# Performance work log

Measured on AMD Instinct MI355X. Metric: run time of the kernel, lower is better.

The kernel has to match this reference:

```python
import jax, jax.numpy as jnp
import numpy as np

DIM = 1024
HEADS = 16
DIM_HEAD = DIM // HEADS  # 64
MAX_FREQ = 256


def rotate_half(x):
    # interleaved pairs: (..., d) -> rotate each (x1, x2) pair to (-x2, x1)
    x = x.reshape(*x.shape[:-1], -1, 2)
    x1, x2 = x[..., 0], x[..., 1]
    return jnp.stack([-x2, x1], axis=-1).reshape(*x.shape[:-2], -1)


def axial_freqs_2d(H, W, rot_dim, max_freq):
    # 'pixel' freqs: linspace(1, max_freq/2, n) * pi per axis; each axis gets rot_dim/2 rotary dims
    n = rot_dim // 4
    freqs = jnp.linspace(1.0, max_freq / 2.0, n, dtype=jnp.float32) * jnp.pi
    ph = jnp.linspace(-1.0, 1.0, H, dtype=jnp.float32)
    pw = jnp.linspace(-1.0, 1.0, W, dtype=jnp.float32)
    fh = jnp.repeat(ph[:, None] * freqs[None, :], 2, axis=-1)  # (H, rot_dim//2)
    fw = jnp.repeat(pw[:, None] * freqs[None, :], 2, axis=-1)  # (W, rot_dim//2)
    fh = jnp.broadcast_to(fh[:, None, :], (H, W, rot_dim // 2))
    fw = jnp.broadcast_to(fw[None, :, :], (H, W, rot_dim // 2))
    return jnp.concatenate([fh, fw], axis=-1)  # (H, W, rot_dim)


def setup_inputs() -> dict:
    key = jax.random.key(0)
    k1, k2, k3 = jax.random.split(key, 3)
    b, H, W = 8, 32, 32
    L = H * W
    x = jax.random.normal(k1, (b, L, DIM), dtype=jnp.float32)
    # torch Linear weights stored pre-transposed for direct x @ W
    w_qkv = jax.random.normal(k2, (DIM, 3 * DIM), dtype=jnp.float32) * (DIM ** -0.5)
    w_proj = jax.random.normal(k3, (DIM, DIM), dtype=jnp.float32) * (DIM ** -0.5)
    return {"x": x, "w_qkv": w_qkv, "w_proj": w_proj, "H": H, "W": W}


def reference(x, w_qkv, w_proj, H, W):
    b, L, d = x.shape
    qkv = x @ w_qkv  # (b, L, 3d)
    q, k, v = jnp.split(qkv, 3, axis=-1)

    def split_heads(t):
        return t.reshape(b, L, HEADS, DIM_HEAD)  # (b, L, h, dh)

    q, k, v = split_heads(q), split_heads(k), split_heads(v)

    # 2D axial RoPE over the full head dim (rope_use_dim == dim_head)
    freqs = axial_freqs_2d(H, W, DIM_HEAD, MAX_FREQ).reshape(L, DIM_HEAD)
    cos = jnp.cos(freqs)[None, :, None, :]  # (1, L, 1, dh)
    sin = jnp.sin(freqs)[None, :, None, :]
    q = q * cos + rotate_half(q) * sin
    k = k * cos + rotate_half(k) * sin

    # module pre-scales q by dh^-0.5 AND SDPA scales again by dh^-0.5 -> dh^-1 total (faithful)
    scale_total = 1.0 / DIM_HEAD
    scores = jnp.einsum('blhd,bmhd->bhlm', q, k) * scale_total  # (b, h, L, L)
    attn = jax.nn.softmax(scores, axis=-1)
    out = jnp.einsum('bhlm,bmhd->blhd', attn, v).reshape(b, L, d)
    return out @ w_proj
```

## Files before the change

kernel.cpp:

```cpp
#include <hip/hip_runtime.h>
#include <hip/hip_bf16.h>
#include <math.h>

typedef __bf16 bf16_t;
typedef __attribute__((ext_vector_type(8))) __bf16 bf16x8;
typedef __attribute__((ext_vector_type(4))) __bf16 bf16x4;
typedef __attribute__((ext_vector_type(4))) short s16x4;
typedef __attribute__((ext_vector_type(4))) float f32x4;

#define AS1C(p) ((const __attribute__((address_space(1))) void*)(p))
#define AS3(p)  ((__attribute__((address_space(3))) void*)(p))

__device__ __forceinline__ float fast_exp2(float x) { return __builtin_amdgcn_exp2f(x); }

__global__ __launch_bounds__(256) void k_cvt(const float* __restrict__ in,
                                             bf16_t* __restrict__ out, int n4) {
    int i = blockIdx.x * 256 + threadIdx.x;
    if (i < n4) {
        float4 v = reinterpret_cast<const float4*>(in)[i];
        bf16x4 o;
        o[0] = (bf16_t)v.x; o[1] = (bf16_t)v.y; o[2] = (bf16_t)v.z; o[3] = (bf16_t)v.w;
        reinterpret_cast<bf16x4*>(out)[i] = o;
    }
}

__global__ __launch_bounds__(256) void k_tconv(const float* __restrict__ in,
                                               bf16_t* __restrict__ out, int R, int C) {
    __shared__ float tile[64][65];
    int r0 = blockIdx.y * 64, c0 = blockIdx.x * 64;
#pragma unroll
    for (int i = 0; i < 16; ++i) {
        int e = i * 256 + threadIdx.x;
        int r = e >> 6, c = e & 63;
        tile[r][c] = in[(size_t)(r0 + r) * C + c0 + c];
    }
    __syncthreads();
#pragma unroll
    for (int i = 0; i < 16; ++i) {
        int e = i * 256 + threadIdx.x;
        int c = e >> 6, r = e & 63;
        out[(size_t)(c0 + c) * R + r0 + r] = (bf16_t)tile[r][c];
    }
}

__global__ __launch_bounds__(256) void k_tab(float* __restrict__ cosT,
                                             float* __restrict__ sinT) {
    int i = blockIdx.x * 256 + threadIdx.x;
    int l = i >> 6, d = i & 63;
    int hh = l >> 5, ww = l & 31;
    float pos = (d < 32) ? (-1.0f + (2.0f / 31.0f) * (float)hh)
                         : (-1.0f + (2.0f / 31.0f) * (float)ww);
    int fi = (d & 31) >> 1;
    float fb = (1.0f + (127.0f / 15.0f) * (float)fi) * 3.14159265358979323846f;
    float fr = pos * fb;
    cosT[i] = cosf(fr);
    sinT[i] = sinf(fr);
}

__device__ __forceinline__ void gemm128_pipe(const bf16_t* __restrict__ A,
                                             const bf16_t* __restrict__ Bt,
                                             int rowA0, int colB0, int w, int l,
                                             bf16_t* As, bf16_t* Bs,
                                             f32x4 acc[4][4]) {
    const int wr = w >> 1, wc = w & 1;
    const int r8 = l >> 3;
    const int sc = ((l & 7) ^ r8) << 3;

#define STG8(buf, kt)                                                                      \
    {                                                                                      \
        _Pragma("unroll")                                                                  \
        for (int j = 0; j < 4; ++j) {                                                      \
            int rr = j * 32 + w * 8 + r8;                                                  \
            __builtin_amdgcn_global_load_lds(                                              \
                AS1C(A + (size_t)(rowA0 + rr) * 1024 + (kt) * 64 + sc),                    \
                AS3(As + (buf) * 8192 + (j * 32 + w * 8) * 64), 16, 0, 0);                 \
            __builtin_amdgcn_global_load_lds(                                              \
                AS1C(Bt + (size_t)(colB0 + rr) * 1024 + (kt) * 64 + sc),                   \
                AS3(Bs + (buf) * 8192 + (j * 32 + w * 8) * 64), 16, 0, 0);                 \
        }                                                                                  \
    }

    STG8(0, 0);
    for (int T = 0; T < 16; ++T) {
        if (T < 15) {
            STG8((T + 1) & 1, T + 1);
            asm volatile("s_waitcnt vmcnt(8)" ::: "memory");
        } else {
            asm volatile("s_waitcnt vmcnt(0)" ::: "memory");
        }
        __builtin_amdgcn_s_barrier();
        const bf16_t* cA = As + (T & 1) * 8192;
        const bf16_t* cB = Bs + (T & 1) * 8192;
#pragma unroll
        for (int kk = 0; kk < 2; ++kk) {
            const int ec = (kk * 32 + (l >> 4) * 8) ^ ((l & 7) << 3);
            bf16x8 af[4], bfr[4];
#pragma unroll
            for (int mm = 0; mm < 4; ++mm)
                af[mm] = *reinterpret_cast<const bf16x8*>(
                    cA + (wr * 64 + mm * 16 + (l & 15)) * 64 + ec);
#pragma unroll
            for (int n = 0; n < 4; ++n)
                bfr[n] = *reinterpret_cast<const bf16x8*>(
                    cB + (wc * 64 + n * 16 + (l & 15)) * 64 + ec);
            asm volatile("s_waitcnt lgkmcnt(0)" ::: "memory");
            __builtin_amdgcn_sched_barrier(0);
            __builtin_amdgcn_s_setprio(1);
#pragma unroll
            for (int mm = 0; mm < 4; ++mm)
#pragma unroll
                for (int n = 0; n < 4; ++n)
                    acc[mm][n] = __builtin_amdgcn_mfma_f32_16x16x32_bf16(af[mm], bfr[n],
                                                                         acc[mm][n], 0, 0, 0);
            __builtin_amdgcn_s_setprio(0);
        }
        __builtin_amdgcn_s_barrier();
    }
#undef STG8
}

__global__ __launch_bounds__(256, 2) void k_gemm_qkv(const bf16_t* __restrict__ A,
                                                     const bf16_t* __restrict__ Bt,
                                                     const float* __restrict__ cosT,
                                                     const float* __restrict__ sinT,
                                                     bf16_t* __restrict__ qb,
                                                     bf16_t* __restrict__ kb,
                                                     bf16_t* __restrict__ vb) {
    __shared__ alignas(128) char smem[65536];
    bf16_t* As = (bf16_t*)smem;
    bf16_t* Bs = (bf16_t*)(smem + 32768);
    const int tid = threadIdx.x, w = tid >> 6, l = tid & 63;
    const int wr = w >> 1, wc = w & 1;
    const int bid = blockIdx.x;
    const int xcd = bid & 7, idx = bid >> 3;
    const int by = (xcd >> 1) * 16 + (idx & 15);
    const int bx = (xcd & 1) * 12 + (idx >> 4);
    const int rowA0 = by * 128, colB0 = bx * 128;

    f32x4 acc[4][4] = {};
    gemm128_pipe(A, Bt, rowA0, colB0, w, l, As, Bs, acc);

    const int part = colB0 >> 10;
    if (part == 2) {
        __builtin_amdgcn_sched_barrier(0);
        __syncthreads();
        bf16_t* Tb = (bf16_t*)smem;
#pragma unroll
        for (int m = 0; m < 4; ++m)
#pragma unroll
            for (int n = 0; n < 4; ++n) {
                int cc = wc * 64 + n * 16 + (l & 15);
                int rr = wr * 64 + m * 16 + (l >> 4) * 4;
#pragma unroll
                for (int r = 0; r < 4; ++r)
                    Tb[cc * 136 + rr + r] = (bf16_t)acc[m][n][r];
            }
        __syncthreads();
        const int j = tid >> 1, half = tid & 1;
        const int c = colB0 + j;
        const int head = (c & 1023) >> 6, d = c & 63;
        const int bb = rowA0 >> 10, ll0 = rowA0 & 1023;
        bf16_t* dst = vb + (((size_t)bb * 16 + head) * 64 + d) * 1024 + ll0 + half * 64;
        const bf16_t* srcp = Tb + j * 136 + half * 64;
#pragma unroll
        for (int e = 0; e < 8; ++e)
            *reinterpret_cast<bf16x8*>(dst + e * 8) =
                *reinterpret_cast<const bf16x8*>(srcp + e * 8);
    } else {
        bf16_t* dstb = (part == 0) ? qb : kb;
#pragma unroll
        for (int m = 0; m < 4; ++m)
#pragma unroll
            for (int n = 0; n < 4; ++n) {
                const int c = colB0 + wc * 64 + n * 16 + (l & 15);
                const int head = (c & 1023) >> 6;
                const int d = c & 63;
                const int rbase = rowA0 + wr * 64 + m * 16 + (l >> 4) * 4;
#pragma unroll
                for (int r = 0; r < 4; ++r) {
                    int row = rbase + r;
                    int bb = row >> 10, ll = row & 1023;
                    float v0 = acc[m][n][r];
                    float vp = __shfl_xor(v0, 1, 64);
                    float cs = cosT[ll * 64 + d];
                    float sn = sinT[ll * 64 + d];
                    float res = (d & 1) ? fmaf(vp, sn, v0 * cs) : fmaf(-vp, sn, v0 * cs);
                    dstb[(((size_t)bb * 16 + head) * 1024 + ll) * 64 + d] = (bf16_t)res;
                }
            }
    }
}

__global__ __launch_bounds__(256, 2) void k_gemm_out(const bf16_t* __restrict__ A,
                                                     const bf16_t* __restrict__ Bt,
                                                     float* __restrict__ out) {
    __shared__ alignas(128) char smem[65536];
    bf16_t* As = (bf16_t*)smem;
    bf16_t* Bs = (bf16_t*)(smem + 32768);
    const int tid = threadIdx.x, w = tid >> 6, l = tid & 63;
    const int wr = w >> 1, wc = w & 1;
    const int bid = blockIdx.x;
    const int xcd = bid & 7, idx = bid >> 3;
    const int by = (xcd >> 1) * 16 + (idx & 15);
    const int bx = (xcd & 1) * 4 + (idx >> 4);
    const int rowA0 = by * 128, colB0 = bx * 128;

    f32x4 acc[4][4] = {};
    gemm128_pipe(A, Bt, rowA0, colB0, w, l, As, Bs, acc);

#pragma unroll
    for (int m = 0; m < 4; ++m)
#pragma unroll
        for (int n = 0; n < 4; ++n) {
            int c = colB0 + wc * 64 + n * 16 + (l & 15);
            int rbase = rowA0 + wr * 64 + m * 16 + (l >> 4) * 4;
#pragma unroll
            for (int r = 0; r < 4; ++r)
                out[(size_t)(rbase + r) * 1024 + c] = acc[m][n][r];
        }
}

__global__ __launch_bounds__(256, 4) void k_attn(const bf16_t* __restrict__ qb,
                                                 const bf16_t* __restrict__ kb,
                                                 const bf16_t* __restrict__ vb,
                                                 bf16_t* __restrict__ ob) {
    __shared__ alignas(128) bf16_t Ks[2][64 * 64];
    __shared__ alignas(128) bf16_t Vs[2][64 * 64];
    const int tid = threadIdx.x, w = tid >> 6, l = tid & 63;
    const int g = l >> 4;
    const int bid = blockIdx.x;
    const int bs = (bid & 7) * 128 + (bid >> 3);
    const int bh = bs >> 3, bi = bh >> 4, h = bh & 15;
    const int q0 = (bs & 7) * 128;
    const bf16_t* qbase = qb + (size_t)bh * 1024 * 64;
    const bf16_t* kbase = kb + (size_t)bh * 1024 * 64;
    const bf16_t* vbase = vb + (size_t)bh * 64 * 1024;

    bf16x8 qf[2][2];
#pragma unroll
    for (int m = 0; m < 2; ++m) {
        int qrow = q0 + m * 64 + w * 16 + (l & 15);
#pragma unroll
        for (int kk = 0; kk < 2; ++kk)
            qf[m][kk] = *reinterpret_cast<const bf16x8*>(
                qbase + (size_t)qrow * 64 + kk * 32 + g * 8);
    }

    float m_run[2] = {-1e30f, -1e30f};
    float l_run[2] = {0.f, 0.f};
    f32x4 o_acc[2][4] = {};

    const int srow = l >> 3;
    const int sc = 8 * ((l & 7) ^ srow);
#define STAGE(buf, kv0)                                                                   \
    {                                                                                     \
        _Pragma("unroll")                                                                 \
        for (int i = 0; i < 2; ++i) {                                                     \
            int rr = (i * 4 + w) * 8 + srow;                                              \
            __builtin_amdgcn_global_load_lds(AS1C(kbase + (size_t)((kv0) + rr) * 64 + sc),\
                                             AS3(&Ks[buf][(i * 4 + w) * 512]), 16, 0, 0); \
            __builtin_amdgcn_global_load_lds(AS1C(vbase + (size_t)rr * 1024 + (kv0) + sc),\
                                             AS3(&Vs[buf][(i * 4 + w) * 512]), 16, 0, 0); \
        }                                                                                 \
    }

    STAGE(0, 0);
    __syncthreads();

    const float SCL = 1.4426950408889634f / 64.0f;
    int cur = 0;
    for (int t = 0; t < 16; ++t) {
        if (t < 15) STAGE(cur ^ 1, (t + 1) * 64);

        f32x4 sacc[2][4] = {};
        __builtin_amdgcn_s_setprio(1);
#pragma unroll
        for (int kk = 0; kk < 2; ++kk)
#pragma unroll
            for (int n = 0; n < 4; ++n) {
                int rr = n * 16 + (l & 15);
                int ec = (kk * 32 + g * 8) ^ ((l & 7) << 3);
                bf16x8 kfr = *reinterpret_cast<const bf16x8*>(&Ks[cur][rr * 64 + ec]);
                sacc[0][n] = __builtin_amdgcn_mfma_f32_16x16x32_bf16(kfr, qf[0][kk], sacc[0][n], 0, 0, 0);
                sacc[1][n] = __builtin_amdgcn_mfma_f32_16x16x32_bf16(kfr, qf[1][kk], sacc[1][n], 0, 0, 0);
            }
        __builtin_amdgcn_s_setprio(0);

        s16x4 pa[2][4];
#pragma unroll
        for (int m = 0; m < 2; ++m) {
            float mxr = -1e30f;
#pragma unroll
            for (int n = 0; n < 4; ++n)
#pragma unroll
                for (int r = 0; r < 4; ++r) mxr = fmaxf(mxr, sacc[m][n][r]);
            mxr = fmaxf(mxr, __shfl_xor(mxr, 16, 64));
            mxr = fmaxf(mxr, __shfl_xor(mxr, 32, 64));
            float mx = mxr * SCL;
            float mo = m_run[m];
            if (__any(mx > mo + 8.0f)) {
                float mn = fmaxf(mo, mx);
                float corr = fast_exp2(mo - mn);
                l_run[m] *= corr;
                m_run[m] = mn; mo = mn;
#pragma unroll
                for (int r = 0; r < 4; ++r) {
                    float c2 = __shfl(corr, (l & 48) | (g * 4 + r), 64);
#pragma unroll
                    for (int n = 0; n < 4; ++n) o_acc[m][n][r] *= c2;
                }
            }
            float lsum = 0.f;
#pragma unroll
            for (int n = 0; n < 4; ++n) {
                bf16x4 pb;
#pragma unroll
                for (int r = 0; r < 4; ++r) {
                    float pv = fast_exp2(fmaf(sacc[m][n][r], SCL, -mo));
                    lsum += pv;
                    pb[r] = (bf16_t)pv;
                }
                pa[m][n] = __builtin_bit_cast(s16x4, pb);
            }
            l_run[m] += lsum;
        }

        const char* vrow = (const char*)&Vs[cur][0] + (l & 15) * 128;
        __builtin_amdgcn_s_setprio(1);
#pragma unroll
        for (int c = 0; c < 4; ++c) {
            int kvb = (c * 32 + g * 8) ^ ((l & 7) << 4);
#pragma unroll
            for (int nd = 0; nd < 4; ++nd) {
                s16x4 vf = *reinterpret_cast<const s16x4*>(vrow + nd * 2048 + kvb);
                o_acc[0][nd] = __builtin_amdgcn_mfma_f32_16x16x16bf16_1k(pa[0][c], vf, o_acc[0][nd], 0, 0, 0);
                o_acc[1][nd] = __builtin_amdgcn_mfma_f32_16x16x16bf16_1k(pa[1][c], vf, o_acc[1][nd], 0, 0, 0);
            }
        }
        __builtin_amdgcn_s_setprio(0);
        __syncthreads();
        cur ^= 1;
    }

#pragma unroll
    for (int m = 0; m < 2; ++m) {
        float ls = l_run[m];
        ls += __shfl_xor(ls, 16, 64);
        ls += __shfl_xor(ls, 32, 64);
        float inv = 1.0f / ls;
#pragma unroll
        for (int r = 0; r < 4; ++r) {
            float c2 = __shfl(inv, (l & 48) | (g * 4 + r), 64);
            int row = q0 + m * 64 + w * 16 + g * 4 + r;
#pragma unroll
            for (int n = 0; n < 4; ++n)
                ob[((size_t)bi * 1024 + row) * 1024 + h * 64 + n * 16 + (l & 15)] =
                    (bf16_t)(o_acc[m][n][r] * c2);
        }
    }
#undef STAGE
}

extern "C" void kernel_launch(void* const* d_in, const int* in_sizes, int n_in,
                              void* d_out, int out_size, void* d_ws, size_t ws_size,
                              hipStream_t stream) {
    (void)in_sizes; (void)n_in; (void)out_size; (void)ws_size;
    const float* x     = (const float*)d_in[0];
    const float* wqkv  = (const float*)d_in[1];
    const float* wproj = (const float*)d_in[2];
    char* ws = (char*)d_ws;

    bf16_t* xb  = (bf16_t*)(ws);
    bf16_t* wqT = (bf16_t*)(ws + 16777216ull);
    bf16_t* wpT = (bf16_t*)(ws + 23068672ull);
    bf16_t* qb  = (bf16_t*)(ws + 25165824ull);
    bf16_t* kb  = (bf16_t*)(ws + 41943040ull);
    bf16_t* vb  = (bf16_t*)(ws + 58720256ull);
    bf16_t* ob  = (bf16_t*)(ws + 75497472ull);
    float*  cosT = (float*)(ws + 92274688ull);
    float*  sinT = (float*)(ws + 92536832ull);

    k_cvt<<<8192, 256, 0, stream>>>(x, xb, 2097152);
    k_tconv<<<dim3(48, 16), 256, 0, stream>>>(wqkv, wqT, 1024, 3072);
    k_tconv<<<dim3(16, 16), 256, 0, stream>>>(wproj, wpT, 1024, 1024);
    k_tab<<<256, 256, 0, stream>>>(cosT, sinT);
    k_gemm_qkv<<<1536, 256, 0, stream>>>(xb, wqT, cosT, sinT, qb, kb, vb);
    k_attn<<<1024, 256, 0, stream>>>(qb, kb, vb, ob);
    k_gemm_out<<<512, 256, 0, stream>>>(ob, wpT, (float*)d_out);
}
```

Before: 167.9 us.

## Merge prep kernels into one launch and enlarge attention blocks to 512 threads

Folds the four preprocessing kernels (x conversion, two weight transposes, rope table) into a single launch that dispatches on block index, cutting launch overhead. The attention kernel now uses 8 waves per block covering 256 query rows, so each staged K/V tile is shared by twice as many queries and each wave issues one load per stage. It also drops the s_setprio hints. Larger blocks mean fewer blocks in the grid and possibly lower occupancy per CU.

```diff
diff --git a/kernel.cpp b/kernel.cpp
--- a/kernel.cpp
+++ b/kernel.cpp
@@ -13,48 +13,58 @@
 
 __device__ __forceinline__ float fast_exp2(float x) { return __builtin_amdgcn_exp2f(x); }
 
-__global__ __launch_bounds__(256) void k_cvt(const float* __restrict__ in,
-                                             bf16_t* __restrict__ out, int n4) {
-    int i = blockIdx.x * 256 + threadIdx.x;
-    if (i < n4) {
-        float4 v = reinterpret_cast<const float4*>(in)[i];
+__device__ __forceinline__ void tconv_body(const float* __restrict__ in,
+                                           bf16_t* __restrict__ out, int R, int C,
+                                           int r0, int c0, float (*tile)[65], int tid) {
+#pragma unroll
+    for (int i = 0; i < 16; ++i) {
+        int e = i * 256 + tid;
+        int r = e >> 6, c = e & 63;
+        tile[r][c] = in[(size_t)(r0 + r) * C + c0 + c];
+    }
+    __syncthreads();
+#pragma unroll
+    for (int i = 0; i < 16; ++i) {
+        int e = i * 256 + tid;
+        int c = e >> 6, r = e & 63;
+        out[(size_t)(c0 + c) * R + r0 + r] = (bf16_t)tile[r][c];
+    }
+}
+
+__global__ __launch_bounds__(256) void k_prep(const float* __restrict__ x,
+                                              const float* __restrict__ wqkv,
+                                              const float* __restrict__ wproj,
+                                              bf16_t* __restrict__ xb,
+                                              bf16_t* __restrict__ wqT,
+                                              bf16_t* __restrict__ wpT,
+                                              float* __restrict__ cosT,
+                                              float* __restrict__ sinT) {
+    __shared__ float tile[64][65];
+    const int bid = blockIdx.x, tid = threadIdx.x;
+    if (bid < 8192) {
+        int i = bid * 256 + tid;
+        float4 v = reinterpret_cast<const float4*>(x)[i];
         bf16x4 o;
         o[0] = (bf16_t)v.x; o[1] = (bf16_t)v.y; o[2] = (bf16_t)v.z; o[3] = (bf16_t)v.w;
-        reinterpret_cast<bf16x4*>(out)[i] = o;
-    }
-}
-
-__global__ __launch_bounds__(256) void k_tconv(const float* __restrict__ in,
-                                               bf16_t* __restrict__ out, int R, int C) {
-    __shared__ float tile[64][65];
-    int r0 = blockIdx.y * 64, c0 = blockIdx.x * 64;
-#pragma unroll
-    for (int i = 0; i < 16; ++i) {
-        int e = i * 256 + threadIdx.x;
-        int r = e >> 6, c = e & 63;
-        tile[r][c] = in[(size_t)(r0 + r) * C + c0 + c];
-    }
-    __syncthreads();
-#pragma unroll
-    for (int i = 0; i < 16; ++i) {
-        int e = i * 256 + threadIdx.x;
-        int c = e >> 6, r = e & 63;
-        out[(size_t)(c0 + c) * R + r0 + r] = (bf16_t)tile[r][c];
-    }
-}
-
-__global__ __launch_bounds__(256) void k_tab(float* __restrict__ cosT,
-                                             float* __restrict__ sinT) {
-    int i = blockIdx.x * 256 + threadIdx.x;
-    int l = i >> 6, d = i & 63;
-    int hh = l >> 5, ww = l & 31;
-    float pos = (d < 32) ? (-1.0f + (2.0f / 31.0f) * (float)hh)
-                         : (-1.0f + (2.0f / 31.0f) * (float)ww);
-    int fi = (d & 31) >> 1;
-    float fb = (1.0f + (127.0f / 15.0f) * (float)fi) * 3.14159265358979323846f;
-    float fr = pos * fb;
-    cosT[i] = cosf(fr);
-    sinT[i] = sinf(fr);
+        reinterpret_cast<bf16x4*>(xb)[i] = o;
+    } else if (bid < 8960) {
+        int t = bid - 8192;
+        tconv_body(wqkv, wqT, 1024, 3072, (t / 48) * 64, (t % 48) * 64, tile, tid);
+    } else if (bid < 9216) {
+        int t = bid - 8960;
+        tconv_body(wproj, wpT, 1024, 1024, (t / 16) * 64, (t % 16) * 64, tile, tid);
+    } else {
+        int i = (bid - 9216) * 256 + tid;
+        int l = i >> 6, d = i & 63;
+        int hh = l >> 5, ww = l & 31;
+        float pos = (d < 32) ? (-1.0f + (2.0f / 31.0f) * (float)hh)
+                             : (-1.0f + (2.0f / 31.0f) * (float)ww);
+        int fi = (d & 31) >> 1;
+        float fb = (1.0f + (127.0f / 15.0f) * (float)fi) * 3.14159265358979323846f;
+        float fr = pos * fb;
+        cosT[i] = cosf(fr);
+        sinT[i] = sinf(fr);
+    }
 }
 
 __device__ __forceinline__ void gemm128_pipe(const bf16_t* __restrict__ A,
@@ -220,7 +230,7 @@
         }
 }
 
-__global__ __launch_bounds__(256, 4) void k_attn(const bf16_t* __restrict__ qb,
+__global__ __launch_bounds__(512, 4) void k_attn(const bf16_t* __restrict__ qb,
                                                  const bf16_t* __restrict__ kb,
                                                  const bf16_t* __restrict__ vb,
                                                  bf16_t* __restrict__ ob) {
@@ -229,9 +239,9 @@
     const int tid = threadIdx.x, w = tid >> 6, l = tid & 63;
     const int g = l >> 4;
     const int bid = blockIdx.x;
-    const int bs = (bid & 7) * 128 + (bid >> 3);
-    const int bh = bs >> 3, bi = bh >> 4, h = bh & 15;
-    const int q0 = (bs & 7) * 128;
+    const int bs = (bid & 7) * 64 + (bid >> 3);
+    const int bh = bs >> 2, bi = bh >> 4, h = bh & 15;
+    const int q0 = (bs & 3) * 256;
     const bf16_t* qbase = qb + (size_t)bh * 1024 * 64;
     const bf16_t* kbase = kb + (size_t)bh * 1024 * 64;
     const bf16_t* vbase = vb + (size_t)bh * 64 * 1024;
@@ -239,7 +249,7 @@
     bf16x8 qf[2][2];
 #pragma unroll
     for (int m = 0; m < 2; ++m) {
-        int qrow = q0 + m * 64 + w * 16 + (l & 15);
+        int qrow = q0 + w * 32 + m * 16 + (l & 15);
 #pragma unroll
         for (int kk = 0; kk < 2; ++kk)
             qf[m][kk] = *reinterpret_cast<const bf16x8*>(
@@ -254,14 +264,11 @@
     const int sc = 8 * ((l & 7) ^ srow);
 #define STAGE(buf, kv0)                                                                   \
     {                                                                                     \
-        _Pragma("unroll")                                                                 \
-        for (int i = 0; i < 2; ++i) {                                                     \
-            int rr = (i * 4 + w) * 8 + srow;                                              \
-            __builtin_amdgcn_global_load_lds(AS1C(kbase + (size_t)((kv0) + rr) * 64 + sc),\
-                                             AS3(&Ks[buf][(i * 4 + w) * 512]), 16, 0, 0); \
-            __builtin_amdgcn_global_load_lds(AS1C(vbase + (size_t)rr * 1024 + (kv0) + sc),\
-                                             AS3(&Vs[buf][(i * 4 + w) * 512]), 16, 0, 0); \
-        }                                                                                 \
+        int rr = w * 8 + srow;                                                            \
+        __builtin_amdgcn_global_load_lds(AS1C(kbase + (size_t)((kv0) + rr) * 64 + sc),    \
+                                         AS3(&Ks[buf][w * 512]), 16, 0, 0);               \
+        __builtin_amdgcn_global_load_lds(AS1C(vbase + (size_t)rr * 1024 + (kv0) + sc),    \
+                                         AS3(&Vs[buf][w * 512]), 16, 0, 0);               \
     }
 
     STAGE(0, 0);
@@ -273,7 +280,6 @@
         if (t < 15) STAGE(cur ^ 1, (t + 1) * 64);
 
         f32x4 sacc[2][4] = {};
-        __builtin_amdgcn_s_setprio(1);
 #pragma unroll
         for (int kk = 0; kk < 2; ++kk)
 #pragma unroll
@@ -284,7 +290,6 @@
                 sacc[0][n] = __builtin_amdgcn_mfma_f32_16x16x32_bf16(kfr, qf[0][kk], sacc[0][n], 0, 0, 0);
                 sacc[1][n] = __builtin_amdgcn_mfma_f32_16x16x32_bf16(kfr, qf[1][kk], sacc[1][n], 0, 0, 0);
             }
-        __builtin_amdgcn_s_setprio(0);
 
         s16x4 pa[2][4];
 #pragma unroll
@@ -326,7 +331,6 @@
         }
 
         const char* vrow = (const char*)&Vs[cur][0] + (l & 15) * 128;
-        __builtin_amdgcn_s_setprio(1);
 #pragma unroll
         for (int c = 0; c < 4; ++c) {
             int kvb = (c * 32 + g * 8) ^ ((l & 7) << 4);
@@ -337,7 +341,6 @@
                 o_acc[1][nd] = __builtin_amdgcn_mfma_f32_16x16x16bf16_1k(pa[1][c], vf, o_acc[1][nd], 0, 0, 0);
             }
         }
-        __builtin_amdgcn_s_setprio(0);
         __syncthreads();
         cur ^= 1;
     }
@@ -351,7 +354,7 @@
 #pragma unroll
         for (int r = 0; r < 4; ++r) {
             float c2 = __shfl(inv, (l & 48) | (g * 4 + r), 64);
-            int row = q0 + m * 64 + w * 16 + g * 4 + r;
+            int row = q0 + w * 32 + m * 16 + g * 4 + r;
 #pragma unroll
             for (int n = 0; n < 4; ++n)
                 ob[((size_t)bi * 1024 + row) * 1024 + h * 64 + n * 16 + (l & 15)] =
@@ -380,11 +383,8 @@
     float*  cosT = (float*)(ws + 92274688ull);
     float*  sinT = (float*)(ws + 92536832ull);
 
-    k_cvt<<<8192, 256, 0, stream>>>(x, xb, 2097152);
-    k_tconv<<<dim3(48, 16), 256, 0, stream>>>(wqkv, wqT, 1024, 3072);
-    k_tconv<<<dim3(16, 16), 256, 0, stream>>>(wproj, wpT, 1024, 1024);
-    k_tab<<<256, 256, 0, stream>>>(cosT, sinT);
+    k_prep<<<9472, 256, 0, stream>>>(x, wqkv, wproj, xb, wqT, wpT, cosT, sinT);
     k_gemm_qkv<<<1536, 256, 0, stream>>>(xb, wqT, cosT, sinT, qb, kb, vb);
-    k_attn<<<1024, 256, 0, stream>>>(qb, kb, vb, ob);
+    k_attn<<<512, 512, 0, stream>>>(qb, kb, vb, ob);
     k_gemm_out<<<512, 256, 0, stream>>>(ob, wpT, (float*)d_out);
 }
```

Result: faster. 154.7 us (-7.9%).
